# Performance work log

Hardware: AMD Instinct MI355X
Metric: run time of the kernel (lower is better)

## Reference

```python
import jax, jax.numpy as jnp
import numpy as np

N = 10000
E = 320000
IN_DIM = 256
HID = 128
HEADS = 3
NEG_SLOPE = 0.2
EPS = 1e-8


def setup_inputs() -> dict:
    key = jax.random.key(0)
    ks = jax.random.split(key, 12)
    rn = lambda k, s, sc=0.1: jax.random.normal(k, s, dtype=jnp.float32) * sc
    return {
        'x1': jax.random.normal(ks[0], (N, IN_DIM), dtype=jnp.float32),
        'edge_index1': jax.random.randint(ks[1], (2, E), 0, N, dtype=jnp.int64),
        'x2': jax.random.normal(ks[2], (N, IN_DIM), dtype=jnp.float32),
        'edge_index2': jax.random.randint(ks[3], (2, E), 0, N, dtype=jnp.int64),
        'W1': rn(ks[4], (IN_DIM, HEADS * HID)),
        'att_src1': rn(ks[5], (HEADS, HID)),
        'att_dst1': rn(ks[6], (HEADS, HID)),
        'b1': rn(ks[7], (HEADS * HID,)),
        'W2': rn(ks[8], (HEADS * HID, HID)),
        'att_src2': rn(ks[9], (1, HID)),
        'att_dst2': rn(ks[10], (1, HID)),
        'b2': rn(ks[11], (HID,)),
    }


def gat_conv(x, edge_index, W, a_src, a_dst, bias, heads, out_ch, concat):
    """PyG-style GATConv with add_self_loops=True."""
    n = x.shape[0]
    loops = jnp.arange(n, dtype=edge_index.dtype)
    ei = jnp.concatenate([edge_index, jnp.stack([loops, loops])], axis=1)
    src, dst = ei[0], ei[1]
    h = (x @ W).reshape(n, heads, out_ch)                    # [N,H,C]
    s = jnp.einsum('nhc,hc->nh', h, a_src)                    # alpha_src per node
    d = jnp.einsum('nhc,hc->nh', h, a_dst)                    # alpha_dst per node
    e = jax.nn.leaky_relu(s[src] + d[dst], NEG_SLOPE)         # [Etot,H]
    m = jax.ops.segment_max(e, dst, num_segments=n)           # segment softmax (stable)
    ex = jnp.exp(e - m[dst])
    denom = jax.ops.segment_sum(ex, dst, num_segments=n)
    alpha = ex / denom[dst]                                   # [Etot,H]
    out = jax.ops.segment_sum(h[src] * alpha[:, :, None], dst, num_segments=n)
    out = out.reshape(n, heads * out_ch) if concat else out.mean(axis=1)
    return out + bias, (ei, alpha)


def _branch(x, ei, W1, as1, ad1, b1, W2, as2, ad2, b2):
    e1, (ei_sl, alpha1) = gat_conv(x, ei, W1, as1, ad1, b1, HEADS, HID, True)
    e1 = jax.nn.relu(e1)
    e2, _ = gat_conv(e1, ei, W2, as2, ad2, b2, 1, HID, False)
    # _graph_pooling
    attn_val = alpha1.mean(axis=1)                            # [Etot]
    node_attn = jax.ops.segment_sum(attn_val, ei_sl[1], num_segments=x.shape[0])
    weighted = e2 * node_attn[:, None]
    pooled = jnp.concatenate([weighted.mean(axis=0), e2.mean(axis=0)])  # [2*HID]
    return pooled, alpha1


def reference(x1, edge_index1, x2, edge_index2, W1, att_src1, att_dst1, b1,
              W2, att_src2, att_dst2, b2):
    g1, alpha1 = _branch(x1, edge_index1, W1, att_src1, att_dst1, b1,
                         W2, att_src2, att_dst2, b2)
    g2, alpha2 = _branch(x2, edge_index2, W1, att_src1, att_dst1, b1,
                         W2, att_src2, att_dst2, b2)
    n1 = jnp.maximum(jnp.linalg.norm(g1), EPS)
    n2 = jnp.maximum(jnp.linalg.norm(g2), EPS)
    sim = jnp.dot(g1, g2) / (n1 * n2)
    return sim, alpha1, alpha2
```

## Files before the change

kernel.cpp:

```cpp
#include <hip/hip_runtime.h>
#include <hip/hip_bf16.h>
#include <cstdint>
#include <cstddef>

#define INDIM 256
#define NEG 0.2f

typedef __attribute__((ext_vector_type(8))) short short8v;
typedef __attribute__((ext_vector_type(4))) float f32x4;
typedef __attribute__((ext_vector_type(2))) float f32x2;

__device__ __forceinline__ unsigned short f2bf(float x) {
  __hip_bfloat16 b = __float2bfloat16(x);
  return __builtin_bit_cast(unsigned short, b);
}

__device__ __forceinline__ unsigned char f2fp8(float v) {
  int packed = __builtin_amdgcn_cvt_pk_fp8_f32(v, v, 0, false);
  return (unsigned char)(packed & 0xff);
}

__device__ __forceinline__ float lrelu(float v) { return v > 0.f ? v : NEG * v; }

__global__ void wprep_kernel(const float* __restrict__ W1, __hip_bfloat16* __restrict__ W1t,
                             const float* __restrict__ W2, __hip_bfloat16* __restrict__ W2t) {
  int idx = blockIdx.x * blockDim.x + threadIdx.x;
  const int T1 = 256 * 384;
  if (idx < T1) {
    int k = idx / 384, c = idx - k * 384;
    W1t[(size_t)c * 256 + k] = __float2bfloat16(W1[idx]);
  } else {
    int i = idx - T1;
    if (i < 384 * 128) {
      int k = i / 128, c = i - k * 128;
      W2t[(size_t)c * 384 + k] = __float2bfloat16(W2[i]);
    }
  }
}

template<int K, bool ABF16, int NH>
__global__ __launch_bounds__(256) void mfma_gemm(const void* __restrict__ A0,
                                                 const void* __restrict__ A1, int Nsplit,
                                                 const __hip_bfloat16* __restrict__ Wt,
                                                 const float* __restrict__ att_s,
                                                 const float* __restrict__ att_d,
                                                 unsigned char* __restrict__ Yc,
                                                 float* __restrict__ So,
                                                 float* __restrict__ Do,
                                                 int M, int NC) {
  __shared__ short As[64][40];
  __shared__ short Bs[128][40];
  __shared__ float sred[2][64];
  const int tid = threadIdx.x;
  const int row0 = blockIdx.x * 64;
  const int col0 = blockIdx.y * 128;
  const int l = tid & 63, w = tid >> 6;
  const int wr = w >> 1, wc = w & 1;
  const int lr = l & 15, lk = (l >> 4) * 8;

  f32x4 acc[2][4];
#pragma unroll
  for (int m = 0; m < 2; ++m)
#pragma unroll
    for (int n = 0; n < 4; ++n) acc[m][n] = {0.f, 0.f, 0.f, 0.f};

  for (int k0 = 0; k0 < K; k0 += 32) {
    __syncthreads();
    {
      int r = tid >> 2, kq = (tid & 3) * 8;
      int gr = row0 + r;
      short8v av = {0, 0, 0, 0, 0, 0, 0, 0};
      if (gr < M) {
        const void* Ab = (gr < Nsplit) ? A0 : A1;
        int lrow = (gr < Nsplit) ? gr : gr - Nsplit;
        if (ABF16) {
          av = *(const short8v*)((const short*)Ab + (size_t)lrow * K + k0 + kq);
        } else {
          const float* ap = (const float*)Ab + (size_t)lrow * K + k0 + kq;
          float4 u = *(const float4*)ap;
          float4 v = *(const float4*)(ap + 4);
          av = short8v{(short)f2bf(u.x), (short)f2bf(u.y), (short)f2bf(u.z), (short)f2bf(u.w),
                       (short)f2bf(v.x), (short)f2bf(v.y), (short)f2bf(v.z), (short)f2bf(v.w)};
        }
      }
      *(short8v*)&As[r][kq] = av;
    }
    {
      int c = tid >> 1, kq = (tid & 1) * 8;
      const short* wp = (const short*)Wt + (size_t)(col0 + c) * K + k0 + kq;
      *(short8v*)&Bs[c][kq]      = *(const short8v*)wp;
      *(short8v*)&Bs[c][kq + 16] = *(const short8v*)(wp + 16);
    }
    __syncthreads();
    short8v a[2], b[4];
#pragma unroll
    for (int m = 0; m < 2; ++m) a[m] = *(short8v*)&As[wr * 32 + m * 16 + lr][lk];
#pragma unroll
    for (int n = 0; n < 4; ++n) b[n] = *(short8v*)&Bs[wc * 64 + n * 16 + lr][lk];
#pragma unroll
    for (int m = 0; m < 2; ++m)
#pragma unroll
      for (int n = 0; n < 4; ++n)
        acc[m][n] = __builtin_amdgcn_mfma_f32_16x16x32_bf16(a[m], b[n], acc[m][n], 0, 0, 0);
  }
#pragma unroll
  for (int m = 0; m < 2; ++m) {
    int rbase = row0 + wr * 32 + m * 16 + (l >> 4) * 4;
#pragma unroll
    for (int n = 0; n < 4; ++n) {
      int col = col0 + wc * 64 + n * 16 + lr;
#pragma unroll
      for (int q = 0; q < 4; ++q) {
        int row = rbase + q;
        if (row < M) Yc[(size_t)row * NC + col] = f2fp8(acc[m][n][q]);
      }
    }
  }
  float asv[4], adv[4];
#pragma unroll
  for (int n = 0; n < 4; ++n) {
    int col = col0 + wc * 64 + n * 16 + lr;
    asv[n] = att_s[col];
    adv[n] = att_d[col];
  }
  float ps[2][4], pd[2][4];
#pragma unroll
  for (int m = 0; m < 2; ++m)
#pragma unroll
    for (int q = 0; q < 4; ++q) {
      float s = 0.f, d = 0.f;
#pragma unroll
      for (int n = 0; n < 4; ++n) {
        s = fmaf(acc[m][n][q], asv[n], s);
        d = fmaf(acc[m][n][q], adv[n], d);
      }
      ps[m][q] = s; pd[m][q] = d;
    }
#pragma unroll
  for (int o = 1; o < 16; o <<= 1) {
#pragma unroll
    for (int m = 0; m < 2; ++m)
#pragma unroll
      for (int q = 0; q < 4; ++q) {
        ps[m][q] += __shfl_xor(ps[m][q], o);
        pd[m][q] += __shfl_xor(pd[m][q], o);
      }
  }
  __syncthreads();
  if (wc == 1 && lr == 0) {
#pragma unroll
    for (int m = 0; m < 2; ++m)
#pragma unroll
      for (int q = 0; q < 4; ++q) {
        int rl = wr * 32 + m * 16 + (l >> 4) * 4 + q;
        sred[0][rl] = ps[m][q];
        sred[1][rl] = pd[m][q];
      }
  }
  __syncthreads();
  if (wc == 0 && lr == 0) {
#pragma unroll
    for (int m = 0; m < 2; ++m)
#pragma unroll
      for (int q = 0; q < 4; ++q) {
        int rl = wr * 32 + m * 16 + (l >> 4) * 4 + q;
        int row = row0 + rl;
        if (row < M) {
          So[(size_t)row * NH + blockIdx.y] = ps[m][q] + sred[0][rl];
          Do[(size_t)row * NH + blockIdx.y] = pd[m][q] + sred[1][rl];
        }
      }
  }
}

__global__ void deg_kernel(const int* __restrict__ ed1, const int* __restrict__ ed2,
                           int E, int Etot, int N, int* __restrict__ deg) {
  int idx = blockIdx.x * blockDim.x + threadIdx.x;
  if (idx >= 2 * Etot) return;
  int br = idx >= Etot;
  int el = idx - br * Etot;
  const int* ed = br ? ed2 : ed1;
  int dn = ((el < E) ? ed[el] : (el - E)) + br * N;
  atomicAdd(&deg[dn], 1);
}

__global__ __launch_bounds__(1024) void scan_kernel(const int* __restrict__ deg,
                                                    int* __restrict__ rowptr,
                                                    int* __restrict__ cursor, int n) {
  __shared__ int wsum[16];
  int t = threadIdx.x, lane = t & 63, wid = t >> 6;
  int start = t * 20;
  int v[20];
  int s = 0;
#pragma unroll
  for (int k = 0; k < 20; ++k) {
    int i = start + k;
    int d = (i < n) ? deg[i] : 0;
    s += d;
    v[k] = s;
  }
  int x = s;
#pragma unroll
  for (int o = 1; o < 64; o <<= 1) {
    int tm = __shfl_up(x, o);
    if (lane >= o) x += tm;
  }
  if (lane == 63) wsum[wid] = x;
  __syncthreads();
  if (wid == 0) {
    int wv = (lane < 16) ? wsum[lane] : 0;
#pragma unroll
    for (int o = 1; o < 16; o <<= 1) {
      int tm = __shfl_up(wv, o);
      if (lane >= o) wv += tm;
    }
    if (lane < 16) wsum[lane] = wv;
  }
  __syncthreads();
  int excl = (x - s) + (wid ? wsum[wid - 1] : 0);
  if (t == 0) rowptr[0] = 0;
#pragma unroll
  for (int k = 0; k < 20; ++k) {
    int i = start + k;
    if (i < n) {
      rowptr[i + 1] = excl + v[k];
      cursor[i] = excl + (k ? v[k - 1] : 0);
    }
  }
}

__global__ void fill_kernel(const int* __restrict__ es1, const int* __restrict__ ed1,
                            const int* __restrict__ es2, const int* __restrict__ ed2,
                            int E, int Etot, int N, int* __restrict__ cursor,
                            int* __restrict__ csr_src) {
  int idx = blockIdx.x * blockDim.x + threadIdx.x;
  if (idx >= 2 * Etot) return;
  int br = idx >= Etot;
  int el = idx - br * Etot;
  const int* es = br ? es2 : es1;
  const int* ed = br ? ed2 : ed1;
  int sn, dn;
  if (el < E) { sn = es[el]; dn = ed[el]; } else { sn = dn = el - E; }
  sn += br * N; dn += br * N;
  int pos = atomicAdd(&cursor[dn], 1);
  csr_src[pos] = sn;
}

__global__ __launch_bounds__(192) void agg1_kernel(const unsigned char* __restrict__ h1c,
                                                   const float* __restrict__ S,
                                                   const float* __restrict__ D,
                                                   const int* __restrict__ rowptr,
                                                   const int* __restrict__ csr_src,
                                                   const float* __restrict__ b1,
                                                   __hip_bfloat16* __restrict__ e1b,
                                                   float* __restrict__ invden) {
  __shared__ int lsrc[192];
  __shared__ float la[3][192];
  __shared__ float red[3][3];
  __shared__ float inv_s[3];
  const unsigned int* H4 = reinterpret_cast<const unsigned int*>(h1c);
  int n = blockIdx.x;
  int j = threadIdx.x;
  int wid = j >> 6, lane = j & 63;
  int half = (j >= 96) ? 1 : 0;
  int t = j - half * 96;
  int head = t >> 5;
  int p0 = rowptr[n], p1 = rowptr[n + 1];
  float d0 = D[n * 3], d1 = D[n * 3 + 1], d2 = D[n * 3 + 2];

  float dp0 = 0.f, dp1 = 0.f, dp2 = 0.f;
  float acc[4] = {0.f, 0.f, 0.f, 0.f};
  for (int base = p0; base < p1; base += 192) {
    int cnt = min(192, p1 - base);
    __syncthreads();
    if (j < cnt) {
      int sn = csr_src[base + j];
      lsrc[j] = sn;
      float e0 = __expf(lrelu(S[sn * 3] + d0));
      float e1 = __expf(lrelu(S[sn * 3 + 1] + d1));
      float e2 = __expf(lrelu(S[sn * 3 + 2] + d2));
      la[0][j] = e0; la[1][j] = e1; la[2][j] = e2;
      dp0 += e0; dp1 += e1; dp2 += e2;
    }
    __syncthreads();
    int i = half;
    for (; i + 14 < cnt; i += 16) {
      unsigned int hv[8];
      float av[8];
#pragma unroll
      for (int u = 0; u < 8; ++u) {
        int e = i + 2 * u;
        int sn = lsrc[e];
        av[u] = la[head][e];
        hv[u] = H4[(size_t)sn * 96 + t];
      }
#pragma unroll
      for (int u = 0; u < 8; ++u) {
        f32x2 f0 = __builtin_amdgcn_cvt_pk_f32_fp8((int)hv[u], false);
        f32x2 f1 = __builtin_amdgcn_cvt_pk_f32_fp8((int)hv[u], true);
        acc[0] = fmaf(av[u], f0.x, acc[0]);
        acc[1] = fmaf(av[u], f0.y, acc[1]);
        acc[2] = fmaf(av[u], f1.x, acc[2]);
        acc[3] = fmaf(av[u], f1.y, acc[3]);
      }
    }
    for (; i < cnt; i += 2) {
      int sn = lsrc[i];
      float a = la[head][i];
      unsigned int hv = H4[(size_t)sn * 96 + t];
      f32x2 f0 = __builtin_amdgcn_cvt_pk_f32_fp8((int)hv, false);
      f32x2 f1 = __builtin_amdgcn_cvt_pk_f32_fp8((int)hv, true);
      acc[0] = fmaf(a, f0.x, acc[0]);
      acc[1] = fmaf(a, f0.y, acc[1]);
      acc[2] = fmaf(a, f1.x, acc[2]);
      acc[3] = fmaf(a, f1.y, acc[3]);
    }
  }
  __syncthreads();
  float* racc = &la[0][0];
  if (half == 1) {
    racc[t * 4 + 0] = acc[0]; racc[t * 4 + 1] = acc[1];
    racc[t * 4 + 2] = acc[2]; racc[t * 4 + 3] = acc[3];
  }
  __syncthreads();
  if (half == 0) {
    acc[0] += racc[t * 4 + 0]; acc[1] += racc[t * 4 + 1];
    acc[2] += racc[t * 4 + 2]; acc[3] += racc[t * 4 + 3];
  }
#pragma unroll
  for (int o = 32; o; o >>= 1) {
    dp0 += __shfl_down(dp0, o); dp1 += __shfl_down(dp1, o); dp2 += __shfl_down(dp2, o);
  }
  if (lane == 0) { red[wid][0] = dp0; red[wid][1] = dp1; red[wid][2] = dp2; }
  __syncthreads();
  if (j == 0) {
    inv_s[0] = 1.f / (red[0][0] + red[1][0] + red[2][0]);
    inv_s[1] = 1.f / (red[0][1] + red[1][1] + red[2][1]);
    inv_s[2] = 1.f / (red[0][2] + red[1][2] + red[2][2]);
  }
  __syncthreads();
  if (half == 0) {
    float inv = inv_s[head];
    float4 bb = *reinterpret_cast<const float4*>(b1 + 4 * t);
    float v0 = acc[0] * inv + bb.x;
    float v1 = acc[1] * inv + bb.y;
    float v2 = acc[2] * inv + bb.z;
    float v3 = acc[3] * inv + bb.w;
    v0 = v0 > 0.f ? v0 : 0.f; v1 = v1 > 0.f ? v1 : 0.f;
    v2 = v2 > 0.f ? v2 : 0.f; v3 = v3 > 0.f ? v3 : 0.f;
    uint2 st;
    st.x = (unsigned int)f2bf(v0) | ((unsigned int)f2bf(v1) << 16);
    st.y = (unsigned int)f2bf(v2) | ((unsigned int)f2bf(v3) << 16);
    *reinterpret_cast<uint2*>(reinterpret_cast<unsigned short*>(e1b) + (size_t)n * 384 + 4 * t) = st;
  }
  if (j < 3) invden[n * 3 + j] = inv_s[j];
}

__global__ void alpha_kernel(const float* __restrict__ S, const float* __restrict__ D,
                             const float* __restrict__ invden,
                             const int* __restrict__ es1, const int* __restrict__ ed1,
                             const int* __restrict__ es2, const int* __restrict__ ed2,
                             int E, int Etot, int N, float* __restrict__ out) {
  int idx = blockIdx.x * blockDim.x + threadIdx.x;
  if (idx >= 2 * Etot) return;
  int br = idx >= Etot;
  int el = idx - br * Etot;
  const int* es = br ? es2 : es1;
  const int* ed = br ? ed2 : ed1;
  int sn, dn;
  if (el < E) { sn = es[el]; dn = ed[el]; } else { sn = dn = el - E; }
  sn += br * N; dn += br * N;
  float* ao = out + 1 + (size_t)br * Etot * 3 + (size_t)el * 3;
#pragma unroll
  for (int h = 0; h < 3; ++h) {
    float v = lrelu(S[sn * 3 + h] + D[dn * 3 + h]);
    ao[h] = __expf(v) * invden[dn * 3 + h];
  }
}

__global__ __launch_bounds__(128) void agg2_kernel(const unsigned char* __restrict__ h2c,
                                                   const float* __restrict__ S2,
                                                   const float* __restrict__ D2,
                                                   const int* __restrict__ rowptr,
                                                   const int* __restrict__ csr_src,
                                                   const float* __restrict__ b2,
                                                   float* __restrict__ e2out, int N2) {
  __shared__ int lsrc[2][256];
  __shared__ float la[2][256];
  const unsigned int* H4 = reinterpret_cast<const unsigned int*>(h2c);
  int wv = threadIdx.x >> 6;
  int n = blockIdx.x * 2 + wv;
  if (n >= N2) return;
  int lane = threadIdx.x & 63;
  int half = lane >> 5, t = lane & 31;
  int p0 = rowptr[n], p1 = rowptr[n + 1];
  float dnv = D2[n];

  float dpart = 0.f;
  float acc[4] = {0.f, 0.f, 0.f, 0.f};
  for (int base = p0; base < p1; base += 256) {
    int cnt = min(256, p1 - base);
    for (int i = lane; i < cnt; i += 64) {
      int sn = csr_src[base + i];
      lsrc[wv][i] = sn;
      float ex = __expf(lrelu(S2[sn] + dnv));
      la[wv][i] = ex;
      dpart += ex;
    }
    int i = half;
    for (; i + 14 < cnt; i += 16) {
      unsigned int hv[8];
      float av[8];
#pragma unroll
      for (int u = 0; u < 8; ++u) {
        int e = i + 2 * u;
        int sn = lsrc[wv][e];
        av[u] = la[wv][e];
        hv[u] = H4[(size_t)sn * 32 + t];
      }
#pragma unroll
      for (int u = 0; u < 8; ++u) {
        f32x2 f0 = __builtin_amdgcn_cvt_pk_f32_fp8((int)hv[u], false);
        f32x2 f1 = __builtin_amdgcn_cvt_pk_f32_fp8((int)hv[u], true);
        acc[0] = fmaf(av[u], f0.x, acc[0]);
        acc[1] = fmaf(av[u], f0.y, acc[1]);
        acc[2] = fmaf(av[u], f1.x, acc[2]);
        acc[3] = fmaf(av[u], f1.y, acc[3]);
      }
    }
    for (; i < cnt; i += 2) {
      int sn = lsrc[wv][i];
      float a = la[wv][i];
      unsigned int hv = H4[(size_t)sn * 32 + t];
      f32x2 f0 = __builtin_amdgcn_cvt_pk_f32_fp8((int)hv, false);
      f32x2 f1 = __builtin_amdgcn_cvt_pk_f32_fp8((int)hv, true);
      acc[0] = fmaf(a, f0.x, acc[0]);
      acc[1] = fmaf(a, f0.y, acc[1]);
      acc[2] = fmaf(a, f1.x, acc[2]);
      acc[3] = fmaf(a, f1.y, acc[3]);
    }
  }
#pragma unroll
  for (int k = 0; k < 4; ++k) acc[k] += __shfl_xor(acc[k], 32);
#pragma unroll
  for (int o = 32; o; o >>= 1) dpart += __shfl_down(dpart, o);
  float invden = 1.f / __shfl(dpart, 0);
  if (half == 0) {
    float4 bb = *reinterpret_cast<const float4*>(b2 + 4 * t);
    float4 ov;
    ov.x = acc[0] * invden + bb.x;
    ov.y = acc[1] * invden + bb.y;
    ov.z = acc[2] * invden + bb.z;
    ov.w = acc[3] * invden + bb.w;
    *reinterpret_cast<float4*>(e2out + (size_t)n * 128 + 4 * t) = ov;
  }
}

__global__ __launch_bounds__(128) void pool_kernel(const float* __restrict__ e2,
                                                   float* __restrict__ g, int N, float invN) {
  int c = threadIdx.x;
  int br = blockIdx.y;
  int r0 = br * N + blockIdx.x * 128;
  int r1 = min(r0 + 128, br * N + N);
  float acc = 0.f;
  for (int n = r0; n < r1; ++n) acc += e2[(size_t)n * 128 + c];
  atomicAdd(&g[br * 128 + c], acc * invN);
}

__global__ __launch_bounds__(128) void sim_kernel(const float* __restrict__ g1,
                                                  const float* __restrict__ g2,
                                                  float* __restrict__ out) {
  int t = threadIdx.x;
  float a = g1[t], b = g2[t];
  __shared__ float sd[128], s1[128], s2[128];
  sd[t] = a * b; s1[t] = a * a; s2[t] = b * b;
  __syncthreads();
  for (int ofs = 64; ofs; ofs >>= 1) {
    if (t < ofs) { sd[t] += sd[t + ofs]; s1[t] += s1[t + ofs]; s2[t] += s2[t + ofs]; }
    __syncthreads();
  }
  if (t == 0) {
    float n1 = fmaxf(sqrtf(s1[0]), 1e-8f);
    float n2 = fmaxf(sqrtf(s2[0]), 1e-8f);
    out[0] = sd[0] / (n1 * n2);
  }
}

extern "C" void kernel_launch(void* const* d_in, const int* in_sizes, int n_in,
                              void* d_out, int out_size, void* d_ws, size_t ws_size,
                              hipStream_t stream) {
  const int N = in_sizes[0] / INDIM;
  const int E = in_sizes[1] / 2;
  const int Etot = E + N;
  const int N2 = 2 * N;

  const float* x1  = (const float*)d_in[0];
  const int*   ei1 = (const int*)d_in[1];
  const float* x2  = (const float*)d_in[2];
  const int*   ei2 = (const int*)d_in[3];
  const float* W1  = (const float*)d_in[4];
  const float* as1 = (const float*)d_in[5];
  const float* ad1 = (const float*)d_in[6];
  const float* b1  = (const float*)d_in[7];
  const float* W2  = (const float*)d_in[8];
  const float* as2 = (const float*)d_in[9];
  const float* ad2 = (const float*)d_in[10];
  const float* b2  = (const float*)d_in[11];
  float* out = (float*)d_out;
  const int* es1 = ei1, *ed1 = ei1 + E;
  const int* es2 = ei2, *ed2 = ei2 + E;

  char* p = (char*)d_ws;
  auto alloc = [&](size_t bytes) -> char* {
    char* q = p;
    p += (bytes + 255) & ~(size_t)255;
    return q;
  };
  unsigned char* h1c = (unsigned char*)alloc((size_t)N2 * 384);
  __hip_bfloat16* e1b = (__hip_bfloat16*)alloc((size_t)N2 * 384 * 2);
  unsigned char* h2c = (unsigned char*)alloc((size_t)N2 * 128);
  float* e2          = (float*)alloc((size_t)N2 * 128 * 4);
  __hip_bfloat16* W1t = (__hip_bfloat16*)alloc((size_t)256 * 384 * 2);
  __hip_bfloat16* W2t = (__hip_bfloat16*)alloc((size_t)384 * 128 * 2);
  float* s1v  = (float*)alloc((size_t)N2 * 3 * 4);
  float* d1v  = (float*)alloc((size_t)N2 * 3 * 4);
  float* s2v  = (float*)alloc((size_t)N2 * 4);
  float* d2v  = (float*)alloc((size_t)N2 * 4);
  float* idn  = (float*)alloc((size_t)N2 * 3 * 4);
  float* g    = (float*)alloc(256 * 4);
  int* deg     = (int*)alloc((size_t)N2 * 4);
  int* rowptr  = (int*)alloc((size_t)(N2 + 1) * 4);
  int* cursor  = (int*)alloc((size_t)N2 * 4);
  int* csr_src = (int*)alloc((size_t)2 * Etot * 4);

  const int EB = 256;
  const int egrid2 = (2 * Etot + EB - 1) / EB;
  const int gmx = (N2 + 63) / 64;

  hipMemsetAsync(g, 0, 256 * 4, stream);
  hipMemsetAsync(deg, 0, (size_t)N2 * 4, stream);
  wprep_kernel<<<(256 * 384 + 384 * 128 + 255) / 256, 256, 0, stream>>>(W1, W1t, W2, W2t);

  deg_kernel<<<egrid2, EB, 0, stream>>>(ed1, ed2, E, Etot, N, deg);
  mfma_gemm<256, false, 3><<<dim3(gmx, 3), 256, 0, stream>>>(x1, x2, N, W1t, as1, ad1,
                                                             h1c, s1v, d1v, N2, 384);
  scan_kernel<<<1, 1024, 0, stream>>>(deg, rowptr, cursor, N2);
  fill_kernel<<<egrid2, EB, 0, stream>>>(es1, ed1, es2, ed2, E, Etot, N, cursor, csr_src);

  agg1_kernel<<<N2, 192, 0, stream>>>(h1c, s1v, d1v, rowptr, csr_src, b1, e1b, idn);

  mfma_gemm<384, true, 1><<<dim3(gmx, 1), 256, 0, stream>>>(e1b, e1b, N2, W2t, as2, ad2,
                                                            h2c, s2v, d2v, N2, 128);
  alpha_kernel<<<egrid2, EB, 0, stream>>>(s1v, d1v, idn, es1, ed1, es2, ed2, E, Etot, N, out);
  agg2_kernel<<<(N2 + 1) / 2, 128, 0, stream>>>(h2c, s2v, d2v, rowptr, csr_src, b2, e2, N2);

  pool_kernel<<<dim3((N + 127) / 128, 2), 128, 0, stream>>>(e2, g, N, 1.f / (float)N);
  sim_kernel<<<1, 128, 0, stream>>>(g, g + 256 / 2, out);
}
```

Before: 247.5 us.

## Use one wavefront per node in layer-1 aggregation with float4-padded attention scores

Layer-1 aggregation moves from one 192-thread block per node to one 64-lane wavefront per node, four nodes per block. Each lane covers four head-0/1 channels and two head-2 channels, and block-level barriers and shared-memory reductions become wave shuffles. Per-node attention scores are padded to a stride of four so the source scores load as one float4, and source index plus exp weights are packed into a shared float4. Layer-2 aggregation also goes to four nodes per block. The cost is less parallelism per high-degree node, a serial edge loop per wave, and a strided 16-bit gather for head-2 channels.

```diff
diff --git a/kernel.cpp b/kernel.cpp
--- a/kernel.cpp
+++ b/kernel.cpp
@@ -48,6 +48,7 @@
                                                  float* __restrict__ So,
                                                  float* __restrict__ Do,
                                                  int M, int NC) {
+  constexpr int SST = (NH == 3) ? 4 : 1;
   __shared__ short As[64][40];
   __shared__ short Bs[128][40];
   __shared__ float sred[2][64];
@@ -166,8 +167,8 @@
         int rl = wr * 32 + m * 16 + (l >> 4) * 4 + q;
         int row = row0 + rl;
         if (row < M) {
-          So[(size_t)row * NH + blockIdx.y] = ps[m][q] + sred[0][rl];
-          Do[(size_t)row * NH + blockIdx.y] = pd[m][q] + sred[1][rl];
+          So[(size_t)row * SST + blockIdx.y] = ps[m][q] + sred[0][rl];
+          Do[(size_t)row * SST + blockIdx.y] = pd[m][q] + sred[1][rl];
         }
       }
   }
@@ -246,117 +247,119 @@
   csr_src[pos] = sn;
 }
 
-__global__ __launch_bounds__(192) void agg1_kernel(const unsigned char* __restrict__ h1c,
-                                                   const float* __restrict__ S,
-                                                   const float* __restrict__ D,
+__global__ __launch_bounds__(256) void agg1_kernel(const unsigned char* __restrict__ h1c,
+                                                   const float* __restrict__ S4,
+                                                   const float* __restrict__ D4,
                                                    const int* __restrict__ rowptr,
                                                    const int* __restrict__ csr_src,
                                                    const float* __restrict__ b1,
                                                    __hip_bfloat16* __restrict__ e1b,
-                                                   float* __restrict__ invden) {
-  __shared__ int lsrc[192];
-  __shared__ float la[3][192];
-  __shared__ float red[3][3];
-  __shared__ float inv_s[3];
-  const unsigned int* H4 = reinterpret_cast<const unsigned int*>(h1c);
-  int n = blockIdx.x;
-  int j = threadIdx.x;
-  int wid = j >> 6, lane = j & 63;
-  int half = (j >= 96) ? 1 : 0;
-  int t = j - half * 96;
-  int head = t >> 5;
+                                                   float* __restrict__ invden, int N2) {
+  __shared__ float4 st[4][64];
+  int wv = threadIdx.x >> 6;
+  int n = blockIdx.x * 4 + wv;
+  if (n >= N2) return;
+  int l = threadIdx.x & 63;
+  int head = l >> 5;
+  const float4* S4v = reinterpret_cast<const float4*>(S4);
   int p0 = rowptr[n], p1 = rowptr[n + 1];
-  float d0 = D[n * 3], d1 = D[n * 3 + 1], d2 = D[n * 3 + 2];
+  float d0 = D4[n * 4], d1 = D4[n * 4 + 1], d2 = D4[n * 4 + 2];
 
   float dp0 = 0.f, dp1 = 0.f, dp2 = 0.f;
-  float acc[4] = {0.f, 0.f, 0.f, 0.f};
-  for (int base = p0; base < p1; base += 192) {
-    int cnt = min(192, p1 - base);
-    __syncthreads();
-    if (j < cnt) {
-      int sn = csr_src[base + j];
-      lsrc[j] = sn;
-      float e0 = __expf(lrelu(S[sn * 3] + d0));
-      float e1 = __expf(lrelu(S[sn * 3 + 1] + d1));
-      float e2 = __expf(lrelu(S[sn * 3 + 2] + d2));
-      la[0][j] = e0; la[1][j] = e1; la[2][j] = e2;
+  float acc[6] = {0.f, 0.f, 0.f, 0.f, 0.f, 0.f};
+  for (int base = p0; base < p1; base += 64) {
+    int cnt = min(64, p1 - base);
+    if (l < cnt) {
+      int sn = csr_src[base + l];
+      float4 sv = S4v[sn];
+      float e0 = __expf(lrelu(sv.x + d0));
+      float e1 = __expf(lrelu(sv.y + d1));
+      float e2 = __expf(lrelu(sv.z + d2));
+      st[wv][l] = make_float4(__int_as_float(sn), e0, e1, e2);
       dp0 += e0; dp1 += e1; dp2 += e2;
     }
-    __syncthreads();
-    int i = half;
-    for (; i + 14 < cnt; i += 16) {
-      unsigned int hv[8];
-      float av[8];
-#pragma unroll
-      for (int u = 0; u < 8; ++u) {
-        int e = i + 2 * u;
-        int sn = lsrc[e];
-        av[u] = la[head][e];
-        hv[u] = H4[(size_t)sn * 96 + t];
-      }
-#pragma unroll
-      for (int u = 0; u < 8; ++u) {
+    int i = 0;
+    for (; i + 4 <= cnt; i += 4) {
+      float4 w[4];
+      unsigned int hv[4];
+      unsigned short gv[4];
+#pragma unroll
+      for (int u = 0; u < 4; ++u) {
+        w[u] = st[wv][i + u];
+        int sn = __float_as_int(w[u].x);
+        const unsigned char* row = h1c + (size_t)sn * 384;
+        hv[u] = *reinterpret_cast<const unsigned int*>(row + 4 * l);
+        gv[u] = *reinterpret_cast<const unsigned short*>(row + 256 + 2 * l);
+      }
+#pragma unroll
+      for (int u = 0; u < 4; ++u) {
+        float alo = head ? w[u].z : w[u].y;
+        float ahi = w[u].w;
         f32x2 f0 = __builtin_amdgcn_cvt_pk_f32_fp8((int)hv[u], false);
         f32x2 f1 = __builtin_amdgcn_cvt_pk_f32_fp8((int)hv[u], true);
-        acc[0] = fmaf(av[u], f0.x, acc[0]);
-        acc[1] = fmaf(av[u], f0.y, acc[1]);
-        acc[2] = fmaf(av[u], f1.x, acc[2]);
-        acc[3] = fmaf(av[u], f1.y, acc[3]);
-      }
-    }
-    for (; i < cnt; i += 2) {
-      int sn = lsrc[i];
-      float a = la[head][i];
-      unsigned int hv = H4[(size_t)sn * 96 + t];
+        f32x2 g0 = __builtin_amdgcn_cvt_pk_f32_fp8((int)(unsigned int)gv[u], false);
+        acc[0] = fmaf(alo, f0.x, acc[0]);
+        acc[1] = fmaf(alo, f0.y, acc[1]);
+        acc[2] = fmaf(alo, f1.x, acc[2]);
+        acc[3] = fmaf(alo, f1.y, acc[3]);
+        acc[4] = fmaf(ahi, g0.x, acc[4]);
+        acc[5] = fmaf(ahi, g0.y, acc[5]);
+      }
+    }
+    for (; i < cnt; ++i) {
+      float4 w = st[wv][i];
+      int sn = __float_as_int(w.x);
+      const unsigned char* row = h1c + (size_t)sn * 384;
+      unsigned int hv = *reinterpret_cast<const unsigned int*>(row + 4 * l);
+      unsigned short gv = *reinterpret_cast<const unsigned short*>(row + 256 + 2 * l);
+      float alo = head ? w.z : w.y;
+      float ahi = w.w;
       f32x2 f0 = __builtin_amdgcn_cvt_pk_f32_fp8((int)hv, false);
       f32x2 f1 = __builtin_amdgcn_cvt_pk_f32_fp8((int)hv, true);
-      acc[0] = fmaf(a, f0.x, acc[0]);
-      acc[1] = fmaf(a, f0.y, acc[1]);
-      acc[2] = fmaf(a, f1.x, acc[2]);
-      acc[3] = fmaf(a, f1.y, acc[3]);
-    }
-  }
-  __syncthreads();
-  float* racc = &la[0][0];
-  if (half == 1) {
-    racc[t * 4 + 0] = acc[0]; racc[t * 4 + 1] = acc[1];
-    racc[t * 4 + 2] = acc[2]; racc[t * 4 + 3] = acc[3];
-  }
-  __syncthreads();
-  if (half == 0) {
-    acc[0] += racc[t * 4 + 0]; acc[1] += racc[t * 4 + 1];
-    acc[2] += racc[t * 4 + 2]; acc[3] += racc[t * 4 + 3];
+      f32x2 g0 = __builtin_amdgcn_cvt_pk_f32_fp8((int)(unsigned int)gv, false);
+      acc[0] = fmaf(alo, f0.x, acc[0]);
+      acc[1] = fmaf(alo, f0.y, acc[1]);
+      acc[2] = fmaf(alo, f1.x, acc[2]);
+      acc[3] = fmaf(alo, f1.y, acc[3]);
+      acc[4] = fmaf(ahi, g0.x, acc[4]);
+      acc[5] = fmaf(ahi, g0.y, acc[5]);
+    }
   }
 #pragma unroll
   for (int o = 32; o; o >>= 1) {
     dp0 += __shfl_down(dp0, o); dp1 += __shfl_down(dp1, o); dp2 += __shfl_down(dp2, o);
   }
-  if (lane == 0) { red[wid][0] = dp0; red[wid][1] = dp1; red[wid][2] = dp2; }
-  __syncthreads();
-  if (j == 0) {
-    inv_s[0] = 1.f / (red[0][0] + red[1][0] + red[2][0]);
-    inv_s[1] = 1.f / (red[0][1] + red[1][1] + red[2][1]);
-    inv_s[2] = 1.f / (red[0][2] + red[1][2] + red[2][2]);
-  }
-  __syncthreads();
-  if (half == 0) {
-    float inv = inv_s[head];
-    float4 bb = *reinterpret_cast<const float4*>(b1 + 4 * t);
-    float v0 = acc[0] * inv + bb.x;
-    float v1 = acc[1] * inv + bb.y;
-    float v2 = acc[2] * inv + bb.z;
-    float v3 = acc[3] * inv + bb.w;
-    v0 = v0 > 0.f ? v0 : 0.f; v1 = v1 > 0.f ? v1 : 0.f;
-    v2 = v2 > 0.f ? v2 : 0.f; v3 = v3 > 0.f ? v3 : 0.f;
-    uint2 st;
-    st.x = (unsigned int)f2bf(v0) | ((unsigned int)f2bf(v1) << 16);
-    st.y = (unsigned int)f2bf(v2) | ((unsigned int)f2bf(v3) << 16);
-    *reinterpret_cast<uint2*>(reinterpret_cast<unsigned short*>(e1b) + (size_t)n * 384 + 4 * t) = st;
-  }
-  if (j < 3) invden[n * 3 + j] = inv_s[j];
-}
-
-__global__ void alpha_kernel(const float* __restrict__ S, const float* __restrict__ D,
+  float inv0 = 1.f / __shfl(dp0, 0);
+  float inv1 = 1.f / __shfl(dp1, 0);
+  float inv2 = 1.f / __shfl(dp2, 0);
+
+  float ilo = head ? inv1 : inv0;
+  int c0 = 4 * l;
+  float4 bb = *reinterpret_cast<const float4*>(b1 + c0);
+  float v0 = acc[0] * ilo + bb.x;
+  float v1 = acc[1] * ilo + bb.y;
+  float v2 = acc[2] * ilo + bb.z;
+  float v3 = acc[3] * ilo + bb.w;
+  v0 = v0 > 0.f ? v0 : 0.f; v1 = v1 > 0.f ? v1 : 0.f;
+  v2 = v2 > 0.f ? v2 : 0.f; v3 = v3 > 0.f ? v3 : 0.f;
+  int ch = 256 + 2 * l;
+  float2 bh = *reinterpret_cast<const float2*>(b1 + ch);
+  float v4 = acc[4] * inv2 + bh.x;
+  float v5 = acc[5] * inv2 + bh.y;
+  v4 = v4 > 0.f ? v4 : 0.f; v5 = v5 > 0.f ? v5 : 0.f;
+  unsigned short* eb = reinterpret_cast<unsigned short*>(e1b) + (size_t)n * 384;
+  uint2 lo;
+  lo.x = (unsigned int)f2bf(v0) | ((unsigned int)f2bf(v1) << 16);
+  lo.y = (unsigned int)f2bf(v2) | ((unsigned int)f2bf(v3) << 16);
+  *reinterpret_cast<uint2*>(eb + c0) = lo;
+  *reinterpret_cast<unsigned int*>(eb + ch) =
+      (unsigned int)f2bf(v4) | ((unsigned int)f2bf(v5) << 16);
+  if (l == 0) invden[n * 3] = inv0;
+  else if (l == 1) invden[n * 3 + 1] = inv1;
+  else if (l == 2) invden[n * 3 + 2] = inv2;
+}
+
+__global__ void alpha_kernel(const float* __restrict__ S4, const float* __restrict__ D4,
                              const float* __restrict__ invden,
                              const int* __restrict__ es1, const int* __restrict__ ed1,
                              const int* __restrict__ es2, const int* __restrict__ ed2,
@@ -373,23 +376,23 @@
   float* ao = out + 1 + (size_t)br * Etot * 3 + (size_t)el * 3;
 #pragma unroll
   for (int h = 0; h < 3; ++h) {
-    float v = lrelu(S[sn * 3 + h] + D[dn * 3 + h]);
+    float v = lrelu(S4[sn * 4 + h] + D4[dn * 4 + h]);
     ao[h] = __expf(v) * invden[dn * 3 + h];
   }
 }
 
-__global__ __launch_bounds__(128) void agg2_kernel(const unsigned char* __restrict__ h2c,
+__global__ __launch_bounds__(256) void agg2_kernel(const unsigned char* __restrict__ h2c,
                                                    const float* __restrict__ S2,
                                                    const float* __restrict__ D2,
                                                    const int* __restrict__ rowptr,
                                                    const int* __restrict__ csr_src,
                                                    const float* __restrict__ b2,
                                                    float* __restrict__ e2out, int N2) {
-  __shared__ int lsrc[2][256];
-  __shared__ float la[2][256];
+  __shared__ int lsrc[4][256];
+  __shared__ float la[4][256];
   const unsigned int* H4 = reinterpret_cast<const unsigned int*>(h2c);
   int wv = threadIdx.x >> 6;
-  int n = blockIdx.x * 2 + wv;
+  int n = blockIdx.x * 4 + wv;
   if (n >= N2) return;
   int lane = threadIdx.x & 63;
   int half = lane >> 5, t = lane & 31;
@@ -522,8 +525,8 @@
   float* e2          = (float*)alloc((size_t)N2 * 128 * 4);
   __hip_bfloat16* W1t = (__hip_bfloat16*)alloc((size_t)256 * 384 * 2);
   __hip_bfloat16* W2t = (__hip_bfloat16*)alloc((size_t)384 * 128 * 2);
-  float* s1v  = (float*)alloc((size_t)N2 * 3 * 4);
-  float* d1v  = (float*)alloc((size_t)N2 * 3 * 4);
+  float* s1v  = (float*)alloc((size_t)N2 * 4 * 4);
+  float* d1v  = (float*)alloc((size_t)N2 * 4 * 4);
   float* s2v  = (float*)alloc((size_t)N2 * 4);
   float* d2v  = (float*)alloc((size_t)N2 * 4);
   float* idn  = (float*)alloc((size_t)N2 * 3 * 4);
@@ -547,13 +550,14 @@
   scan_kernel<<<1, 1024, 0, stream>>>(deg, rowptr, cursor, N2);
   fill_kernel<<<egrid2, EB, 0, stream>>>(es1, ed1, es2, ed2, E, Etot, N, cursor, csr_src);
 
-  agg1_kernel<<<N2, 192, 0, stream>>>(h1c, s1v, d1v, rowptr, csr_src, b1, e1b, idn);
+  agg1_kernel<<<(N2 + 3) / 4, 256, 0, stream>>>(h1c, s1v, d1v, rowptr, csr_src, b1,
+                                                e1b, idn, N2);
 
   mfma_gemm<384, true, 1><<<dim3(gmx, 1), 256, 0, stream>>>(e1b, e1b, N2, W2t, as2, ad2,
                                                             h2c, s2v, d2v, N2, 128);
   alpha_kernel<<<egrid2, EB, 0, stream>>>(s1v, d1v, idn, es1, ed1, es2, ed2, E, Etot, N, out);
-  agg2_kernel<<<(N2 + 1) / 2, 128, 0, stream>>>(h2c, s2v, d2v, rowptr, csr_src, b2, e2, N2);
+  agg2_kernel<<<(N2 + 3) / 4, 256, 0, stream>>>(h2c, s2v, d2v, rowptr, csr_src, b2, e2, N2);
 
   pool_kernel<<<dim3((N + 127) / 128, 2), 128, 0, stream>>>(e2, g, N, 1.f / (float)N);
-  sim_kernel<<<1, 128, 0, stream>>>(g, g + 256 / 2, out);
-}
+  sim_kernel<<<1, 128, 0, stream>>>(g, g + 128, out);
+}
```

Result: faster. 234.5 us (-5.3%).
